# Performance work log

Measured on AMD Instinct MI355X. Metric: run time of the kernel, lower is better.

The kernel has to match this reference:

```python
import jax, jax.numpy as jnp
import numpy as np

# MoELoRA dims
B, S, D = 4, 4096, 1024          # batch, seq, in_features
OUT = 3072                       # out_features (merged qkv)
R, E, G = 8, 8, 2                # lora rank, num experts, num enabled groups (q,v)
OD = OUT // 3                    # out channels per group
SCALING = 16.0 / 8.0             # lora_alpha / r


def setup_inputs() -> dict:
    key = jax.random.key(0)
    k0, k1, k2, k3 = jax.random.split(key, 4)
    x = jax.random.normal(k0, (B, S, D), dtype=jnp.float32)
    # routing linear weight [E, D] (nn.Linear stores [out, in])
    W_route = jax.random.normal(k1, (E, D), dtype=jnp.float32) * 0.02
    # per-expert lora_A reshaped to [E, G, R, D] (rows are group-major: G blocks of R)
    A = jax.random.normal(k2, (E, G, R, D), dtype=jnp.float32) * 0.02
    # per-expert lora_B reshaped to [E, G, OD, R] (grouped conv1d weight, kernel=1)
    Bw = jax.random.normal(k3, (E, G, OD, R), dtype=jnp.float32) * 0.02
    # enabled output columns: groups 0 (q) and 2 (v) of the 3-way split
    lora_ind = jnp.concatenate([jnp.arange(OD), jnp.arange(2 * OD, 3 * OD)]).astype(jnp.int64)
    return {"x": x, "W_route": W_route, "A": A, "Bw": Bw, "lora_ind": lora_ind}


def reference(x, W_route, A, Bw, lora_ind):
    # route_weight = softmax(x @ W_route^T) over experts  -> [B,S,E]
    route = jax.nn.softmax(jnp.einsum("bsd,ed->bse", x, W_route), axis=-1)
    # per-expert down-projection: F.linear(x, lora_A)  -> [B,S,E,G,R]
    h = jnp.einsum("bsd,egrd->bsegr", x, A)
    # route weighting commutes with the (linear) up-projection; weight h first
    # to avoid materializing the [B,S,E,G,OD] per-expert outputs.
    wh = h * route[..., None, None]                      # [B,S,E,G,R]
    # grouped conv1d (kernel=1) == per-group matmul; sum over experts
    compact = jnp.einsum("bsegr,egor->bsgo", wh, Bw) * SCALING   # [B,S,G,OD]
    compact = compact.reshape(B, S, G * OD)
    # zero_pad: scatter compact channels into enabled output columns
    out = jnp.zeros((B, S, OUT), dtype=compact.dtype).at[..., lora_ind].set(compact)
    return out
```

## Files before the change

### kernel.cpp

```cpp
#include <hip/hip_runtime.h>
#include <math.h>

#define NTOK   16384
#define DDIM   1024
#define NE     8
#define NF     128
#define FP     144
#define ODIM   1024
#define NOUT   3072
#define SCALE  2.0f
#define TOKB   32

typedef __attribute__((ext_vector_type(8))) short bf16x8;
typedef __attribute__((ext_vector_type(4))) float f32x4;

#define WS_ABT 0
#define WS_BBT 294912

__device__ inline unsigned f2bf(float a, float b) {
    union { float f; unsigned u; } ua, ub;
    ua.f = a; ub.f = b;
    unsigned x = ua.u + (0x7fffu + ((ua.u >> 16) & 1));
    unsigned y = ub.u + (0x7fffu + ((ub.u >> 16) & 1));
    return (x >> 16) | (y & 0xffff0000u);
}

__global__ __launch_bounds__(256) void k_prep(const float* __restrict__ A,
                                              const float* __restrict__ Wr,
                                              const float* __restrict__ Bw,
                                              unsigned short* __restrict__ Abt,
                                              unsigned short* __restrict__ Bbt) {
    const int b = blockIdx.x, t = threadIdx.x;
    if (b < FP) {
        const int col = t * 4;
        float4 v = {0.f, 0.f, 0.f, 0.f};
        if (b < NF)           v = *(const float4*)(A + (size_t)b * DDIM + col);
        else if (b < NF + NE) v = *(const float4*)(Wr + (size_t)(b - NF) * DDIM + col);
        uint2 p; p.x = f2bf(v.x, v.y); p.y = f2bf(v.z, v.w);
        *(uint2*)(Abt + (size_t)b * DDIM + col) = p;
    } else {
        const int idx = (b - FP) * 1024 + t * 4;
        const int g = idx >> 16, o = (idx >> 6) & 1023, er = idx & 63;
        const int e = er >> 3, r0 = er & 7;
        float4 v = *(const float4*)(Bw + ((size_t)(e * 2 + g) * ODIM + o) * 8 + r0);
        uint2 p; p.x = f2bf(v.x, v.y); p.y = f2bf(v.z, v.w);
        *(uint2*)(Bbt + idx) = p;
    }
}

__global__ __launch_bounds__(256) void k_fused(const float* __restrict__ x,
                                               const unsigned short* __restrict__ Abt,
                                               const unsigned short* __restrict__ Bbt,
                                               float* __restrict__ out) {
    __shared__ __align__(16) char smem[45056];
    unsigned short* xs = (unsigned short*)smem;
    unsigned short* ab = (unsigned short*)(smem + 8192);
    float* whs = (float*)smem;

    const int t    = threadIdx.x;
    const int tokb = blockIdx.x * TOKB;
    const int lane = t & 63, w = t >> 6;
    const int m    = w >> 1, h = w & 1;
    const int l15  = lane & 15, lq = lane >> 4;

    f32x4 acc[5];
#pragma unroll
    for (int n = 0; n < 5; ++n) acc[n] = (f32x4){0.f, 0.f, 0.f, 0.f};

    const int xtok = t >> 3;
    const int xc   = t & 7;
    float4 xr[2];

    auto LDX = [&](int k0) {
        xr[0] = *(const float4*)(x + (size_t)(tokb + xtok) * DDIM + k0 + xc * 8);
        xr[1] = *(const float4*)(x + (size_t)(tokb + xtok) * DDIM + k0 + xc * 8 + 4);
    };
    auto WRX = [&](int buf) {
        unsigned short* xb = xs + buf * (TOKB * 64);
        uint4 p;
        p.x = f2bf(xr[0].x, xr[0].y); p.y = f2bf(xr[0].z, xr[0].w);
        p.z = f2bf(xr[1].x, xr[1].y); p.w = f2bf(xr[1].z, xr[1].w);
        const int c8 = xc ^ (xtok & 7);
        *(uint4*)(xb + xtok * 64 + c8 * 8) = p;
    };
    auto LDA = [&](int buf, int k0) {
        unsigned short* base = ab + buf * (144 * 64);
#pragma unroll
        for (int i = 0; i < 5; ++i) {
            if (i < 4 || t < 128) {
                const int c   = i * 256 + t;
                const int row = c >> 3;
                const int c8  = (c & 7) ^ (row & 7);
                const unsigned short* gp = Abt + (size_t)row * DDIM + k0 + c8 * 8;
                unsigned short* lp = base + (i * 256 + w * 64) * 8;
                __builtin_amdgcn_global_load_lds(
                    (const __attribute__((address_space(1))) unsigned int*)gp,
                    (__attribute__((address_space(3))) unsigned int*)lp, 16, 0, 0);
            }
        }
    };

    LDX(0);
    LDA(0, 0);
    WRX(0);
    for (int s = 0; s < 16; ++s) {
        const int cur = s & 1;
        __syncthreads();
        if (s < 15) { LDX((s + 1) * 64); LDA(cur ^ 1, (s + 1) * 64); }
        const unsigned short* xb  = xs + cur * (TOKB * 64);
        const unsigned short* abc = ab + cur * (144 * 64);
#pragma unroll
        for (int ks = 0; ks < 2; ++ks) {
            const int sw = (((ks << 2) | lq) ^ (l15 & 7)) * 8;
            bf16x8 af = *(const bf16x8*)(xb + (m * 16 + l15) * 64 + sw);
#pragma unroll
            for (int j = 0; j < 4; ++j) {
                const int nt = 2 * j + h;
                bf16x8 bf = *(const bf16x8*)(abc + (nt * 16 + l15) * 64 + sw);
                acc[j] = __builtin_amdgcn_mfma_f32_16x16x32_bf16(af, bf, acc[j], 0, 0, 0);
            }
            bf16x8 bl = *(const bf16x8*)(abc + (8 * 16 + l15) * 64 + sw);
            acc[4] = __builtin_amdgcn_mfma_f32_16x16x32_bf16(af, bl, acc[4], 0, 0, 0);
        }
        if (s < 15) WRX(cur ^ 1);
    }

    float mx[4], pv[4], sm[4], rt[4];
#pragma unroll
    for (int r = 0; r < 4; ++r) mx[r] = acc[4][r];
#pragma unroll
    for (int msk = 1; msk <= 4; msk <<= 1)
#pragma unroll
        for (int r = 0; r < 4; ++r) mx[r] = fmaxf(mx[r], __shfl_xor(mx[r], msk, 16));
#pragma unroll
    for (int r = 0; r < 4; ++r) { pv[r] = expf(acc[4][r] - mx[r]); sm[r] = pv[r]; }
#pragma unroll
    for (int msk = 1; msk <= 4; msk <<= 1)
#pragma unroll
        for (int r = 0; r < 4; ++r) sm[r] += __shfl_xor(sm[r], msk, 16);
#pragma unroll
    for (int r = 0; r < 4; ++r) rt[r] = SCALE * pv[r] / sm[r];

    __syncthreads();

#pragma unroll
    for (int j = 0; j < 4; ++j) {
        const int e = 2 * j + h;
        float rb[4];
#pragma unroll
        for (int r = 0; r < 4; ++r) rb[r] = __shfl(rt[r], e, 16);
#pragma unroll
        for (int r = 0; r < 4; ++r)
            whs[(m * 16 + lq * 4 + r) * 140 + e * 16 + l15] = acc[j][r] * rb[r];
    }
    __syncthreads();

    bf16x8 paf[2];
#pragma unroll
    for (int ks = 0; ks < 2; ++ks) {
        const float* hp = whs + (m * 16 + l15) * 140 + ((ks << 2) | lq) * 16 + (h << 3);
        f32x4 v0 = *(const f32x4*)hp;
        f32x4 v1 = *(const f32x4*)(hp + 4);
        uint4 pk;
        pk.x = f2bf(v0[0], v0[1]); pk.y = f2bf(v0[2], v0[3]);
        pk.z = f2bf(v1[0], v1[1]); pk.w = f2bf(v1[2], v1[3]);
        paf[ks] = *(bf16x8*)&pk;
    }
    __syncthreads();

    float* tile = (float*)smem + w * (16 * 132);
    const int erow  = lane >> 5;
    const int ec4   = lane & 31;
    const int gcolb = h << 11;
    const int zcolb = 1024 + (h << 9);
    const float4 zf4 = {0.f, 0.f, 0.f, 0.f};
#pragma unroll 1
    for (int cb = 0; cb < 8; ++cb) {
#pragma unroll
        for (int nn = 0; nn < 8; ++nn) {
            const int n = cb * 8 + nn;
            const unsigned short* bp =
                Bbt + ((size_t)(h << 10) + (n << 4) + l15) * 64 + (lq << 3);
            bf16x8 b0 = *(const bf16x8*)bp;
            bf16x8 b1 = *(const bf16x8*)(bp + 32);
            f32x4 c = {0.f, 0.f, 0.f, 0.f};
            c = __builtin_amdgcn_mfma_f32_16x16x32_bf16(paf[0], b0, c, 0, 0, 0);
            c = __builtin_amdgcn_mfma_f32_16x16x32_bf16(paf[1], b1, c, 0, 0, 0);
#pragma unroll
            for (int r = 0; r < 4; ++r)
                tile[(lq * 4 + r) * 132 + nn * 16 + l15] = c[r];
        }
#pragma unroll
        for (int j = 0; j < 8; ++j) {
            const int row = j * 2 + erow;
            float4 v = *(const float4*)&tile[row * 132 + ec4 * 4];
            *(float4*)(out + (size_t)(tokb + m * 16 + row) * NOUT
                       + gcolb + cb * 128 + ec4 * 4) = v;
        }
#pragma unroll
        for (int i = 0; i < 4; ++i) {
            const int local = i * 64 + lane;
            const int row = cb * 2 + (local >> 7);
            const int c4  = local & 127;
            *(float4*)(out + (size_t)(tokb + m * 16 + row) * NOUT
                       + zcolb + c4 * 4) = zf4;
        }
    }
}

extern "C" void kernel_launch(void* const* d_in, const int* in_sizes, int n_in,
                              void* d_out, int out_size, void* d_ws, size_t ws_size,
                              hipStream_t stream) {
    const float* x  = (const float*)d_in[0];
    const float* Wr = (const float*)d_in[1];
    const float* A  = (const float*)d_in[2];
    const float* Bw = (const float*)d_in[3];
    unsigned short* Abt = (unsigned short*)((char*)d_ws + WS_ABT);
    unsigned short* Bbt = (unsigned short*)((char*)d_ws + WS_BBT);
    float* out = (float*)d_out;

    k_prep <<<FP + 128, 256, 0, stream>>>(A, Wr, Bw, Abt, Bbt);
    k_fused<<<NTOK / TOKB, 256, 0, stream>>>(x, Abt, Bbt, out);
}
```

Measured before the change: 64.53 us.

## Triple-buffer x and A tiles with explicit vmcnt waits and raw barriers

Changes the down-projection K loop from double to triple buffering, prefetching two stages ahead for both the x registers and the async global-to-LDS loads of A. The __syncthreads call is replaced with hand-counted s_waitcnt vmcnt values that differ by wave, because waves 0-1 issue five A loads instead of four. It also adds sched_barriers, a fully unrolled loop and setprio around the MFMA section. The goal is to hide global load latency. In exchange it uses more LDS, which can lower occupancy, and the hand-set wait counts are fragile if the compiler reorders or adds memory operations.

```diff
diff --git a/kernel.cpp b/kernel.cpp
--- a/kernel.cpp
+++ b/kernel.cpp
@@ -52,9 +52,9 @@
                                                const unsigned short* __restrict__ Abt,
                                                const unsigned short* __restrict__ Bbt,
                                                float* __restrict__ out) {
-    __shared__ __align__(16) char smem[45056];
+    __shared__ __align__(16) char smem[67584];
     unsigned short* xs = (unsigned short*)smem;
-    unsigned short* ab = (unsigned short*)(smem + 8192);
+    unsigned short* ab = (unsigned short*)(smem + 12288);
     float* whs = (float*)smem;
 
     const int t    = threadIdx.x;
@@ -69,17 +69,17 @@
 
     const int xtok = t >> 3;
     const int xc   = t & 7;
-    float4 xr[2];
-
-    auto LDX = [&](int k0) {
-        xr[0] = *(const float4*)(x + (size_t)(tokb + xtok) * DDIM + k0 + xc * 8);
-        xr[1] = *(const float4*)(x + (size_t)(tokb + xtok) * DDIM + k0 + xc * 8 + 4);
+    float4 xr[3][2];
+
+    auto LDX = [&](int set, int k0) {
+        xr[set][0] = *(const float4*)(x + (size_t)(tokb + xtok) * DDIM + k0 + xc * 8);
+        xr[set][1] = *(const float4*)(x + (size_t)(tokb + xtok) * DDIM + k0 + xc * 8 + 4);
     };
-    auto WRX = [&](int buf) {
-        unsigned short* xb = xs + buf * (TOKB * 64);
+    auto WRX = [&](int j) {
+        unsigned short* xb = xs + j * (TOKB * 64);
         uint4 p;
-        p.x = f2bf(xr[0].x, xr[0].y); p.y = f2bf(xr[0].z, xr[0].w);
-        p.z = f2bf(xr[1].x, xr[1].y); p.w = f2bf(xr[1].z, xr[1].w);
+        p.x = f2bf(xr[j][0].x, xr[j][0].y); p.y = f2bf(xr[j][0].z, xr[j][0].w);
+        p.z = f2bf(xr[j][1].x, xr[j][1].y); p.w = f2bf(xr[j][1].z, xr[j][1].w);
         const int c8 = xc ^ (xtok & 7);
         *(uint4*)(xb + xtok * 64 + c8 * 8) = p;
     };
@@ -100,15 +100,24 @@
         }
     };
 
-    LDX(0);
-    LDA(0, 0);
+    LDX(0, 0);   LDA(0, 0);
+    LDX(1, 64);  LDA(1, 64);
     WRX(0);
+
+#pragma unroll 16
     for (int s = 0; s < 16; ++s) {
-        const int cur = s & 1;
-        __syncthreads();
-        if (s < 15) { LDX((s + 1) * 64); LDA(cur ^ 1, (s + 1) * 64); }
-        const unsigned short* xb  = xs + cur * (TOKB * 64);
-        const unsigned short* abc = ab + cur * (144 * 64);
+        if (s == 15)    asm volatile("s_waitcnt vmcnt(0)" ::: "memory");
+        else if (w < 2) asm volatile("s_waitcnt vmcnt(7)" ::: "memory");
+        else            asm volatile("s_waitcnt vmcnt(6)" ::: "memory");
+        asm volatile("s_waitcnt lgkmcnt(0)" ::: "memory");
+        __builtin_amdgcn_sched_barrier(0);
+        __builtin_amdgcn_s_barrier();
+        __builtin_amdgcn_sched_barrier(0);
+        if (s + 2 < 16) { LDX((s + 2) % 3, (s + 2) * 64); LDA((s + 2) % 3, (s + 2) * 64); }
+        __builtin_amdgcn_sched_barrier(0);
+        const unsigned short* xb  = xs + (s % 3) * (TOKB * 64);
+        const unsigned short* abc = ab + (s % 3) * (144 * 64);
+        __builtin_amdgcn_s_setprio(1);
 #pragma unroll
         for (int ks = 0; ks < 2; ++ks) {
             const int sw = (((ks << 2) | lq) ^ (l15 & 7)) * 8;
@@ -122,7 +131,8 @@
             bf16x8 bl = *(const bf16x8*)(abc + (8 * 16 + l15) * 64 + sw);
             acc[4] = __builtin_amdgcn_mfma_f32_16x16x32_bf16(af, bl, acc[4], 0, 0, 0);
         }
-        if (s < 15) WRX(cur ^ 1);
+        __builtin_amdgcn_s_setprio(0);
+        if (s + 1 < 16) WRX((s + 1) % 3);
     }
 
     float mx[4], pv[4], sm[4], rt[4];
```

Result: faster. 62.53 us, median of 3 (-3.1%).
